# Kernel optimization log

Hardware: AMD Instinct MI355X
Metric: run time of the kernel (lower is better)

## Reference

```python
import jax, jax.numpy as jnp
import numpy as np

DIM = 768
HEADS = 12
HEAD_DIM = DIM // HEADS


def setup_inputs() -> dict:
    key = jax.random.key(0)
    ks = jax.random.split(key, 5)
    B, N = 2, 2048
    x = jax.random.normal(ks[0], (B, N, DIM), dtype=jnp.float32)
    s = 1.0 / np.sqrt(DIM)
    qkv_w = jax.random.normal(ks[1], (3 * DIM, DIM), dtype=jnp.float32) * s
    qkv_b = jnp.zeros((3 * DIM,), dtype=jnp.float32)
    proj_w = jax.random.normal(ks[2], (DIM, DIM), dtype=jnp.float32) * s
    proj_b = jnp.zeros((DIM,), dtype=jnp.float32)
    return {"x": x, "qkv_w": qkv_w, "qkv_b": qkv_b, "proj_w": proj_w, "proj_b": proj_b}


def reference(x, qkv_w, qkv_b, proj_w, proj_b):
    B, N, C = x.shape
    scale = HEAD_DIM ** -0.5
    qkv = x @ qkv_w.T + qkv_b                      # [B,N,3C]
    qkv = qkv.reshape(B, N, 3, HEADS, HEAD_DIM)
    q = qkv[:, :, 0].transpose(0, 2, 1, 3)         # [B,H,N,D]
    k = qkv[:, :, 1].transpose(0, 2, 1, 3)
    v = qkv[:, :, 2].transpose(0, 2, 1, 3)
    attn = jnp.einsum('bhnd,bhmd->bhnm', q, k) * scale
    attn = jax.nn.softmax(attn, axis=-1)
    out = jnp.einsum('bhnm,bhmd->bhnd', attn, v)   # [B,H,N,D]
    out = out.transpose(0, 2, 1, 3).reshape(B, N, C)
    return out @ proj_w.T + proj_b
```

## Files before the change

### kernel.cpp

```cpp
#include <hip/hip_runtime.h>
#include <hip/hip_bf16.h>

typedef __bf16 bf16x8 __attribute__((ext_vector_type(8)));
typedef float f32x4 __attribute__((ext_vector_type(4)));
typedef float f32x16 __attribute__((ext_vector_type(16)));

#define SEQ   2048
#define NHEAD 12
#define NBH   24
#define QSCALE 0.18033688011112042f

#define CP16(g, l) __builtin_amdgcn_global_load_lds( \
    (const __attribute__((address_space(1))) unsigned int*)(g), \
    (__attribute__((address_space(3))) unsigned int*)(l), 16, 0, 0)

__device__ __forceinline__ unsigned short f2bf(float f) {
  unsigned int u = __builtin_bit_cast(unsigned int, f);
  u += 0x7FFFu + ((u >> 16) & 1u);
  return (unsigned short)(u >> 16);
}
__device__ __forceinline__ unsigned int packbf2_trunc(float lo, float hi) {
  return __builtin_amdgcn_perm(__builtin_bit_cast(unsigned int, hi),
                               __builtin_bit_cast(unsigned int, lo), 0x07060302u);
}
__device__ __forceinline__ float vmax16(const f32x16& s) {
  float a = fmaxf(fmaxf(s[0], s[1]), fmaxf(s[2], s[3]));
  float b = fmaxf(fmaxf(s[4], s[5]), fmaxf(s[6], s[7]));
  float c = fmaxf(fmaxf(s[8], s[9]), fmaxf(s[10], s[11]));
  float d = fmaxf(fmaxf(s[12], s[13]), fmaxf(s[14], s[15]));
  return fmaxf(fmaxf(a, b), fmaxf(c, d));
}

#define NX4  786432
#define NW14 442368
__global__ __launch_bounds__(256) void cvt3_kernel(const float4* __restrict__ x,
                                                   const float4* __restrict__ w1,
                                                   const float4* __restrict__ w2,
                                                   ushort4* __restrict__ xo,
                                                   ushort4* __restrict__ w1o,
                                                   ushort4* __restrict__ w2o) {
  int i = blockIdx.x * 256 + threadIdx.x;
  const float4* s;
  ushort4* d;
  int j = i;
  if (i < NX4)               { s = x;  d = xo; }
  else if (i < NX4 + NW14)   { s = w1; d = w1o; j = i - NX4; }
  else                       { s = w2; d = w2o; j = i - (NX4 + NW14); }
  float4 v = s[j];
  ushort4 r;
  r.x = f2bf(v.x); r.y = f2bf(v.y); r.z = f2bf(v.z); r.w = f2bf(v.w);
  d[j] = r;
}

template <int BM, int BN, int MODE>
__global__ __launch_bounds__(256) void gemm_kernel(const unsigned short* __restrict__ X,
                                                   const unsigned short* __restrict__ W,
                                                   const float* __restrict__ bias,
                                                   unsigned short* __restrict__ Qb,
                                                   unsigned short* __restrict__ Kb,
                                                   unsigned short* __restrict__ Vtb,
                                                   float* __restrict__ Out) {
  constexpr int K = 768, BK = 64;
  constexpr int WM = BM / 2, WN = BN / 2;
  constexpr int MT = WM / 16, NT = WN / 16;
  __shared__ __align__(16) unsigned short Xs[BM * BK];
  __shared__ __align__(16) unsigned short Ws[BN * BK];

  const int tid = threadIdx.x;
  const int w = tid >> 6, lane = tid & 63, quad = lane >> 4, m16 = lane & 15;
  const int wm = w & 1, wn = w >> 1;
  const int row0 = blockIdx.y * BM, col0 = blockIdx.x * BN;

  f32x4 acc[MT][NT];
#pragma unroll
  for (int mt = 0; mt < MT; ++mt)
#pragma unroll
    for (int nt = 0; nt < NT; ++nt) acc[mt][nt] = (f32x4){0.f, 0.f, 0.f, 0.f};

  for (int k0 = 0; k0 < K; k0 += BK) {
    __syncthreads();
#pragma unroll
    for (int j = 0; j < BM / 32; ++j) {
      int e = tid + 256 * j, r = e >> 3, c8 = e & 7;
      CP16(X + (size_t)(row0 + r) * 768 + k0 + ((c8 ^ (r & 7)) << 3), Xs + e * 8);
    }
#pragma unroll
    for (int j = 0; j < BN / 32; ++j) {
      int e = tid + 256 * j, r = e >> 3, c8 = e & 7;
      CP16(W + (size_t)(col0 + r) * 768 + k0 + ((c8 ^ (r & 7)) << 3), Ws + e * 8);
    }
    __syncthreads();
#pragma unroll
    for (int ks = 0; ks < 2; ++ks) {
      const int sw = ((quad + 4 * ks) ^ (m16 & 7)) << 3;
      bf16x8 a[MT], b[NT];
#pragma unroll
      for (int mt = 0; mt < MT; ++mt)
        a[mt] = *(const bf16x8*)(Xs + (wm * WM + mt * 16 + m16) * BK + sw);
#pragma unroll
      for (int nt = 0; nt < NT; ++nt)
        b[nt] = *(const bf16x8*)(Ws + (wn * WN + nt * 16 + m16) * BK + sw);
#pragma unroll
      for (int mt = 0; mt < MT; ++mt)
#pragma unroll
        for (int nt = 0; nt < NT; ++nt)
          acc[mt][nt] = __builtin_amdgcn_mfma_f32_16x16x32_bf16(a[mt], b[nt], acc[mt][nt], 0, 0, 0);
    }
  }

#pragma unroll
  for (int mt = 0; mt < MT; ++mt) {
#pragma unroll
    for (int nt = 0; nt < NT; ++nt) {
      const int m0 = row0 + wm * WM + mt * 16 + quad * 4;
      const int c = col0 + wn * WN + nt * 16 + m16;
      const float bia = bias[c];
      f32x4 v = acc[mt][nt];
      if constexpr (MODE == 0) {
        const int bidx = m0 >> 11, ns = m0 & 2047;
        if (c < 1536) {
          unsigned short* dst;
          float sc;
          int cc;
          if (c < 768) { cc = c; dst = Qb; sc = QSCALE; }
          else         { cc = c - 768; dst = Kb; sc = 1.0f; }
          const int h = cc >> 6, d = cc & 63;
          unsigned short* p = dst + ((size_t)(bidx * NHEAD + h) * SEQ + ns) * 64 + d;
          p[0]   = f2bf((v[0] + bia) * sc);
          p[64]  = f2bf((v[1] + bia) * sc);
          p[128] = f2bf((v[2] + bia) * sc);
          p[192] = f2bf((v[3] + bia) * sc);
        } else {
          const int cc = c - 1536, h = cc >> 6, d = cc & 63;
          const int ns2 = (ns & ~12) | ((ns & 4) << 1) | ((ns & 8) >> 1);
          ushort4 pk;
          pk.x = f2bf(v[0] + bia); pk.y = f2bf(v[1] + bia);
          pk.z = f2bf(v[2] + bia); pk.w = f2bf(v[3] + bia);
          *(ushort4*)(Vtb + ((size_t)(bidx * NHEAD + h) * 64 + d) * SEQ + ns2) = pk;
        }
      } else {
        float* o = Out + (size_t)m0 * 768 + c;
        o[0]       = v[0] + bia;
        o[768]     = v[1] + bia;
        o[2 * 768] = v[2] + bia;
        o[3 * 768] = v[3] + bia;
      }
    }
  }
}

__global__ __launch_bounds__(128, 1) void attn_kernel(const unsigned short* __restrict__ Qb,
                                                      const unsigned short* __restrict__ Kb,
                                                      const unsigned short* __restrict__ Vtb,
                                                      unsigned short* __restrict__ Ab) {
  __shared__ __align__(16) unsigned short S[4][64 * 64];

  const int tid = threadIdx.x;
  const int w = tid >> 6, lane = tid & 63, hi = lane >> 5, l32 = lane & 31;
  const int bh = blockIdx.x % NBH, qt = blockIdx.x / NBH;
  const int bb = bh / NHEAD, h = bh % NHEAD;
  const int q0 = qt * 64 + w * 32;

  const unsigned short* Qp = Qb + (size_t)bh * SEQ * 64;
  const unsigned short* Kp = Kb + (size_t)bh * SEQ * 64;
  const unsigned short* Vp = Vtb + (size_t)bh * 64 * SEQ;

  bf16x8 qf[4];
#pragma unroll
  for (int dc = 0; dc < 4; ++dc)
    qf[dc] = *(const bf16x8*)(Qp + (size_t)(q0 + l32) * 64 + dc * 16 + hi * 8);

  const unsigned short* dsb[2][4];
#pragma unroll
  for (int t32 = 0; t32 < 2; ++t32)
#pragma unroll
    for (int c = 0; c < 4; ++c)
      dsb[t32][c] = &S[0][(t32 * 32 + l32) * 64 + ((((c << 1) | hi) ^ (l32 & 7)) << 3)];

  int koff[4], voff[4];
#pragma unroll
  for (int j = 0; j < 4; ++j) {
    const int e = tid + 128 * j, r = e >> 3, sw = ((e & 7) ^ (r & 7)) << 3;
    koff[j] = r * 64 + sw;
    voff[j] = r * SEQ + sw;
  }
  const int edst = tid * 8;

#pragma unroll
  for (int j = 0; j < 4; ++j) {
    CP16(Kp + koff[j], &S[0][edst + 1024 * j]);
    CP16(Vp + voff[j], &S[2][edst + 1024 * j]);
  }

  f32x16 o[2] = {};
  float m_i = -3.0e38f, l_i = 0.f;
  const unsigned short* Kt = Kp + 4096;
  const unsigned short* Vt = Vp + 64;

#pragma unroll 2
  for (int kt = 0; kt < 32; ++kt) {
    const int cur = kt & 1;
    __syncthreads();

    bf16x8 kf[2][4], vf[2][4];
#pragma unroll
    for (int t32 = 0; t32 < 2; ++t32)
#pragma unroll
      for (int c = 0; c < 4; ++c)
        kf[t32][c] = *(const bf16x8*)(dsb[t32][c] + cur * 4096);
#pragma unroll
    for (int dt = 0; dt < 2; ++dt)
#pragma unroll
      for (int c = 0; c < 4; ++c)
        vf[dt][c] = *(const bf16x8*)(dsb[dt][c] + 8192 + cur * 4096);

    if (kt < 31) {
#pragma unroll
      for (int j = 0; j < 4; ++j) {
        CP16(Kt + koff[j], &S[1 - cur][edst + 1024 * j]);
        CP16(Vt + voff[j], &S[3 - cur][edst + 1024 * j]);
      }
    }
    Kt += 4096;
    Vt += 64;

    __builtin_amdgcn_s_setprio(1);
    f32x16 st[2];
#pragma unroll
    for (int t32 = 0; t32 < 2; ++t32) {
      f32x16 s = {};
#pragma unroll
      for (int dc = 0; dc < 4; ++dc)
        s = __builtin_amdgcn_mfma_f32_32x32x16_bf16(kf[t32][dc], qf[dc], s, 0, 0, 0);
      st[t32] = s;
    }
    __builtin_amdgcn_s_setprio(0);

    float tmax = fmaxf(vmax16(st[0]), vmax16(st[1]));
    tmax = fmaxf(tmax, __shfl_xor(tmax, 32));
    const float mnew = fmaxf(m_i, tmax);
    const float alpha = __builtin_amdgcn_exp2f(m_i - mnew);
    unsigned int pf[2][8];
    float ts[2];
#pragma unroll
    for (int t32 = 0; t32 < 2; ++t32) {
      float pv[16];
#pragma unroll
      for (int e = 0; e < 16; ++e) pv[e] = __builtin_amdgcn_exp2f(st[t32][e] - mnew);
#pragma unroll
      for (int e2 = 0; e2 < 8; ++e2)
        pf[t32][e2] = packbf2_trunc(pv[2 * e2], pv[2 * e2 + 1]);
      const float a = (pv[0] + pv[1]) + (pv[2] + pv[3]);
      const float b = (pv[4] + pv[5]) + (pv[6] + pv[7]);
      const float c = (pv[8] + pv[9]) + (pv[10] + pv[11]);
      const float d = (pv[12] + pv[13]) + (pv[14] + pv[15]);
      ts[t32] = (a + b) + (c + d);
    }
    float ssum = ts[0] + ts[1];
    ssum += __shfl_xor(ssum, 32);
    l_i = l_i * alpha + ssum;
    m_i = mnew;
    o[0] *= alpha;
    o[1] *= alpha;

    __builtin_amdgcn_s_setprio(1);
#pragma unroll
    for (int t32 = 0; t32 < 2; ++t32) {
#pragma unroll
      for (int hh = 0; hh < 2; ++hh) {
        bf16x8 pfrag = __builtin_bit_cast(bf16x8,
            make_uint4(pf[t32][hh * 4], pf[t32][hh * 4 + 1], pf[t32][hh * 4 + 2], pf[t32][hh * 4 + 3]));
        const int cc = 2 * t32 + hh;
#pragma unroll
        for (int dt = 0; dt < 2; ++dt)
          o[dt] = __builtin_amdgcn_mfma_f32_32x32x16_bf16(vf[dt][cc], pfrag, o[dt], 0, 0, 0);
      }
    }
    __builtin_amdgcn_s_setprio(0);
  }

  const float rl = __builtin_amdgcn_rcpf(l_i);
  unsigned short* base = Ab + ((size_t)bb * SEQ + q0 + l32) * 768 + h * 64;
#pragma unroll
  for (int dt = 0; dt < 2; ++dt) {
#pragma unroll
    for (int run = 0; run < 4; ++run) {
      ushort4 pk;
      pk.x = f2bf(o[dt][run * 4 + 0] * rl);
      pk.y = f2bf(o[dt][run * 4 + 1] * rl);
      pk.z = f2bf(o[dt][run * 4 + 2] * rl);
      pk.w = f2bf(o[dt][run * 4 + 3] * rl);
      *(ushort4*)(base + dt * 32 + run * 8 + hi * 4) = pk;
    }
  }
}

extern "C" void kernel_launch(void* const* d_in, const int* in_sizes, int n_in,
                              void* d_out, int out_size, void* d_ws, size_t ws_size,
                              hipStream_t stream) {
  const float* x      = (const float*)d_in[0];
  const float* qkv_w  = (const float*)d_in[1];
  const float* qkv_b  = (const float*)d_in[2];
  const float* proj_w = (const float*)d_in[3];
  const float* proj_b = (const float*)d_in[4];
  float* out = (float*)d_out;

  unsigned short* xb  = (unsigned short*)d_ws;
  unsigned short* wqb = xb + 3145728;
  unsigned short* wpb = wqb + 1769472;
  unsigned short* Qb  = wpb + 589824;
  unsigned short* Kb  = Qb + 3145728;
  unsigned short* Vtb = Kb + 3145728;
  unsigned short* Ab  = Vtb + 3145728;

  cvt3_kernel<<<5376, 256, 0, stream>>>((const float4*)x, (const float4*)qkv_w, (const float4*)proj_w,
                                        (ushort4*)xb, (ushort4*)wqb, (ushort4*)wpb);
  gemm_kernel<128, 96, 0><<<dim3(24, 32), 256, 0, stream>>>(xb, wqb, qkv_b, Qb, Kb, Vtb, nullptr);
  attn_kernel<<<768, 128, 0, stream>>>(Qb, Kb, Vtb, Ab);
  gemm_kernel<64, 96, 1><<<dim3(8, 64), 256, 0, stream>>>(Ab, wpb, proj_b, nullptr, nullptr, nullptr, out);
}
```

Measured before the change: 171.7 us.

## Split attention over key halves into single-wave blocks with a combine kernel

The attention kernel now launches four times as many one-wave blocks. Each block processes 32 queries against half of the key sequence and reads K and V fragments straight from global memory instead of staging them through double-buffered LDS with barriers. Each half writes an unnormalized bf16 partial output plus its running max and sum, and a new combine kernel merges the two halves with rescaling. The aim is higher occupancy and more parallel work for the attention stage. In exchange it adds an extra kernel launch, extra global traffic for the partials, redundant per-wave K/V loads that now depend on cache hits, and an extra bf16 rounding of the intermediates.

```diff
diff --git a/kernel.cpp b/kernel.cpp
--- a/kernel.cpp
+++ b/kernel.cpp
@@ -18,6 +18,9 @@
   unsigned int u = __builtin_bit_cast(unsigned int, f);
   u += 0x7FFFu + ((u >> 16) & 1u);
   return (unsigned short)(u >> 16);
+}
+__device__ __forceinline__ float bfu2f(unsigned int lo16_as_hi) {
+  return __builtin_bit_cast(float, lo16_as_hi);
 }
 __device__ __forceinline__ unsigned int packbf2_trunc(float lo, float hi) {
   return __builtin_amdgcn_perm(__builtin_bit_cast(unsigned int, hi),
@@ -149,80 +152,45 @@
   }
 }
 
-__global__ __launch_bounds__(128, 1) void attn_kernel(const unsigned short* __restrict__ Qb,
-                                                      const unsigned short* __restrict__ Kb,
-                                                      const unsigned short* __restrict__ Vtb,
-                                                      unsigned short* __restrict__ Ab) {
-  __shared__ __align__(16) unsigned short S[4][64 * 64];
-
-  const int tid = threadIdx.x;
-  const int w = tid >> 6, lane = tid & 63, hi = lane >> 5, l32 = lane & 31;
-  const int bh = blockIdx.x % NBH, qt = blockIdx.x / NBH;
+__global__ __launch_bounds__(64) void attn_kernel(const unsigned short* __restrict__ Qb,
+                                                  const unsigned short* __restrict__ Kb,
+                                                  const unsigned short* __restrict__ Vtb,
+                                                  unsigned short* __restrict__ O0,
+                                                  unsigned short* __restrict__ O1,
+                                                  float2* __restrict__ ml) {
+  const int lane = threadIdx.x, hi = lane >> 5, l32 = lane & 31;
+  const int bh = blockIdx.x % NBH;
+  const int rest = blockIdx.x / NBH;
+  const int qt = rest & 63, half = rest >> 6;
   const int bb = bh / NHEAD, h = bh % NHEAD;
-  const int q0 = qt * 64 + w * 32;
+  const int q0 = qt * 32;
 
   const unsigned short* Qp = Qb + (size_t)bh * SEQ * 64;
-  const unsigned short* Kp = Kb + (size_t)bh * SEQ * 64;
-  const unsigned short* Vp = Vtb + (size_t)bh * 64 * SEQ;
-
   bf16x8 qf[4];
 #pragma unroll
   for (int dc = 0; dc < 4; ++dc)
     qf[dc] = *(const bf16x8*)(Qp + (size_t)(q0 + l32) * 64 + dc * 16 + hi * 8);
 
-  const unsigned short* dsb[2][4];
-#pragma unroll
-  for (int t32 = 0; t32 < 2; ++t32)
-#pragma unroll
-    for (int c = 0; c < 4; ++c)
-      dsb[t32][c] = &S[0][(t32 * 32 + l32) * 64 + ((((c << 1) | hi) ^ (l32 & 7)) << 3)];
-
-  int koff[4], voff[4];
-#pragma unroll
-  for (int j = 0; j < 4; ++j) {
-    const int e = tid + 128 * j, r = e >> 3, sw = ((e & 7) ^ (r & 7)) << 3;
-    koff[j] = r * 64 + sw;
-    voff[j] = r * SEQ + sw;
-  }
-  const int edst = tid * 8;
-
-#pragma unroll
-  for (int j = 0; j < 4; ++j) {
-    CP16(Kp + koff[j], &S[0][edst + 1024 * j]);
-    CP16(Vp + voff[j], &S[2][edst + 1024 * j]);
-  }
+  const int kt0 = half * 16;
+  const unsigned short* k0p = Kb + (size_t)bh * SEQ * 64 + (size_t)(kt0 * 64 + l32) * 64 + hi * 8;
+  const unsigned short* k1p = k0p + 32 * 64;
+  const unsigned short* v0p = Vtb + (size_t)bh * 64 * SEQ + (size_t)l32 * SEQ + kt0 * 64 + hi * 8;
+  const unsigned short* v1p = v0p + (size_t)32 * SEQ;
 
   f32x16 o[2] = {};
   float m_i = -3.0e38f, l_i = 0.f;
-  const unsigned short* Kt = Kp + 4096;
-  const unsigned short* Vt = Vp + 64;
 
 #pragma unroll 2
-  for (int kt = 0; kt < 32; ++kt) {
-    const int cur = kt & 1;
-    __syncthreads();
-
+  for (int kt = 0; kt < 16; ++kt) {
     bf16x8 kf[2][4], vf[2][4];
 #pragma unroll
-    for (int t32 = 0; t32 < 2; ++t32)
-#pragma unroll
-      for (int c = 0; c < 4; ++c)
-        kf[t32][c] = *(const bf16x8*)(dsb[t32][c] + cur * 4096);
-#pragma unroll
-    for (int dt = 0; dt < 2; ++dt)
-#pragma unroll
-      for (int c = 0; c < 4; ++c)
-        vf[dt][c] = *(const bf16x8*)(dsb[dt][c] + 8192 + cur * 4096);
-
-    if (kt < 31) {
-#pragma unroll
-      for (int j = 0; j < 4; ++j) {
-        CP16(Kt + koff[j], &S[1 - cur][edst + 1024 * j]);
-        CP16(Vt + voff[j], &S[3 - cur][edst + 1024 * j]);
-      }
-    }
-    Kt += 4096;
-    Vt += 64;
+    for (int c = 0; c < 4; ++c) {
+      kf[0][c] = *(const bf16x8*)(k0p + c * 16);
+      kf[1][c] = *(const bf16x8*)(k1p + c * 16);
+      vf[0][c] = *(const bf16x8*)(v0p + c * 16);
+      vf[1][c] = *(const bf16x8*)(v1p + c * 16);
+    }
+    k0p += 4096; k1p += 4096; v0p += 64; v1p += 64;
 
     __builtin_amdgcn_s_setprio(1);
     f32x16 st[2];
@@ -240,59 +208,92 @@
     tmax = fmaxf(tmax, __shfl_xor(tmax, 32));
     const float mnew = fmaxf(m_i, tmax);
     const float alpha = __builtin_amdgcn_exp2f(m_i - mnew);
-    unsigned int pf[2][8];
+    m_i = mnew;
+    l_i *= alpha;
+    o[0] *= alpha;
+    o[1] *= alpha;
+
     float ts[2];
 #pragma unroll
     for (int t32 = 0; t32 < 2; ++t32) {
       float pv[16];
 #pragma unroll
       for (int e = 0; e < 16; ++e) pv[e] = __builtin_amdgcn_exp2f(st[t32][e] - mnew);
+      unsigned int pf[8];
 #pragma unroll
       for (int e2 = 0; e2 < 8; ++e2)
-        pf[t32][e2] = packbf2_trunc(pv[2 * e2], pv[2 * e2 + 1]);
+        pf[e2] = packbf2_trunc(pv[2 * e2], pv[2 * e2 + 1]);
       const float a = (pv[0] + pv[1]) + (pv[2] + pv[3]);
       const float b = (pv[4] + pv[5]) + (pv[6] + pv[7]);
       const float c = (pv[8] + pv[9]) + (pv[10] + pv[11]);
       const float d = (pv[12] + pv[13]) + (pv[14] + pv[15]);
       ts[t32] = (a + b) + (c + d);
-    }
-    float ssum = ts[0] + ts[1];
-    ssum += __shfl_xor(ssum, 32);
-    l_i = l_i * alpha + ssum;
-    m_i = mnew;
-    o[0] *= alpha;
-    o[1] *= alpha;
-
-    __builtin_amdgcn_s_setprio(1);
-#pragma unroll
-    for (int t32 = 0; t32 < 2; ++t32) {
+      __builtin_amdgcn_s_setprio(1);
 #pragma unroll
       for (int hh = 0; hh < 2; ++hh) {
         bf16x8 pfrag = __builtin_bit_cast(bf16x8,
-            make_uint4(pf[t32][hh * 4], pf[t32][hh * 4 + 1], pf[t32][hh * 4 + 2], pf[t32][hh * 4 + 3]));
+            make_uint4(pf[hh * 4], pf[hh * 4 + 1], pf[hh * 4 + 2], pf[hh * 4 + 3]));
         const int cc = 2 * t32 + hh;
 #pragma unroll
         for (int dt = 0; dt < 2; ++dt)
           o[dt] = __builtin_amdgcn_mfma_f32_32x32x16_bf16(vf[dt][cc], pfrag, o[dt], 0, 0, 0);
       }
-    }
-    __builtin_amdgcn_s_setprio(0);
-  }
-
-  const float rl = __builtin_amdgcn_rcpf(l_i);
-  unsigned short* base = Ab + ((size_t)bb * SEQ + q0 + l32) * 768 + h * 64;
+      __builtin_amdgcn_s_setprio(0);
+    }
+    float ssum = ts[0] + ts[1];
+    ssum += __shfl_xor(ssum, 32);
+    l_i += ssum;
+  }
+
+  unsigned short* base = (half ? O1 : O0) + ((size_t)bb * SEQ + q0 + l32) * 768 + h * 64;
 #pragma unroll
   for (int dt = 0; dt < 2; ++dt) {
 #pragma unroll
     for (int run = 0; run < 4; ++run) {
       ushort4 pk;
-      pk.x = f2bf(o[dt][run * 4 + 0] * rl);
-      pk.y = f2bf(o[dt][run * 4 + 1] * rl);
-      pk.z = f2bf(o[dt][run * 4 + 2] * rl);
-      pk.w = f2bf(o[dt][run * 4 + 3] * rl);
+      pk.x = f2bf(o[dt][run * 4 + 0]);
+      pk.y = f2bf(o[dt][run * 4 + 1]);
+      pk.z = f2bf(o[dt][run * 4 + 2]);
+      pk.w = f2bf(o[dt][run * 4 + 3]);
       *(ushort4*)(base + dt * 32 + run * 8 + hi * 4) = pk;
     }
   }
+  if (hi == 0)
+    ml[(size_t)half * (NBH * SEQ) + bh * SEQ + q0 + l32] = make_float2(m_i, l_i);
+}
+
+__global__ __launch_bounds__(256) void combine_kernel(unsigned short* __restrict__ O0,
+                                                      const unsigned short* __restrict__ O1,
+                                                      const float2* __restrict__ ml) {
+  const int gid = blockIdx.x * 256 + threadIdx.x;
+  const int t = gid / 48, ci = gid - t * 48;
+  const int ch0 = ci * 16, h = ch0 >> 6;
+  const int mlrow = ((t >> 11) * NHEAD + h) * SEQ + (t & 2047);
+  const float2 ml0 = ml[mlrow], ml1 = ml[NBH * SEQ + mlrow];
+  const float m = fmaxf(ml0.x, ml1.x);
+  const float a0 = __builtin_amdgcn_exp2f(ml0.x - m);
+  const float a1 = __builtin_amdgcn_exp2f(ml1.x - m);
+  const float rl = __builtin_amdgcn_rcpf(a0 * ml0.y + a1 * ml1.y);
+  const float s0 = a0 * rl, s1 = a1 * rl;
+  unsigned short* p0 = O0 + (size_t)t * 768 + ch0;
+  const unsigned short* p1 = O1 + (size_t)t * 768 + ch0;
+  uint4 x[2], y[2];
+  x[0] = *(const uint4*)p0;       x[1] = *(const uint4*)(p0 + 8);
+  y[0] = *(const uint4*)p1;       y[1] = *(const uint4*)(p1 + 8);
+#pragma unroll
+  for (int q = 0; q < 2; ++q) {
+    unsigned int* xu = (unsigned int*)&x[q];
+    const unsigned int* yu = (const unsigned int*)&y[q];
+#pragma unroll
+    for (int e = 0; e < 4; ++e) {
+      const unsigned int u0 = xu[e], u1 = yu[e];
+      const float lo = bfu2f(u0 << 16) * s0 + bfu2f(u1 << 16) * s1;
+      const float hi = bfu2f(u0 & 0xFFFF0000u) * s0 + bfu2f(u1 & 0xFFFF0000u) * s1;
+      xu[e] = ((unsigned int)f2bf(hi) << 16) | f2bf(lo);
+    }
+  }
+  *(uint4*)p0 = x[0];
+  *(uint4*)(p0 + 8) = x[1];
 }
 
 extern "C" void kernel_launch(void* const* d_in, const int* in_sizes, int n_in,
@@ -316,6 +317,7 @@
   cvt3_kernel<<<5376, 256, 0, stream>>>((const float4*)x, (const float4*)qkv_w, (const float4*)proj_w,
                                         (ushort4*)xb, (ushort4*)wqb, (ushort4*)wpb);
   gemm_kernel<128, 96, 0><<<dim3(24, 32), 256, 0, stream>>>(xb, wqb, qkv_b, Qb, Kb, Vtb, nullptr);
-  attn_kernel<<<768, 128, 0, stream>>>(Qb, Kb, Vtb, Ab);
+  attn_kernel<<<3072, 64, 0, stream>>>(Qb, Kb, Vtb, Ab, xb, (float2*)wqb);
+  combine_kernel<<<768, 256, 0, stream>>>(Ab, xb, (const float2*)wqb);
   gemm_kernel<64, 96, 1><<<dim3(8, 64), 256, 0, stream>>>(Ab, wpb, proj_b, nullptr, nullptr, nullptr, out);
 }
```

New measurement: 213.1 us. 1.24x slower.

## Split attention KV range in halves, double queries per wave, add combine kernel

Applied to the files above, without the earlier changes.

Each attention wave now handles 64 query rows (two 32-row sub-tiles) that share the same K/V fragments loaded from LDS, halving LDS traffic per query. Work is split along the key dimension into two halves, keeping the block count at 768. Each half writes unnormalized bf16 partial outputs plus per-row (max, sum) to repurposed workspace buffers. A new combine kernel merges the halves with log-sum-exp rescaling. Occupancy is hinted at two blocks per CU. The cost is an extra kernel pass over two activation-sized buffers, higher register pressure, and an added bf16 rounding of unnormalized partials.

```diff
diff --git a/kernel.cpp b/kernel.cpp
--- a/kernel.cpp
+++ b/kernel.cpp
@@ -18,6 +18,9 @@
   unsigned int u = __builtin_bit_cast(unsigned int, f);
   u += 0x7FFFu + ((u >> 16) & 1u);
   return (unsigned short)(u >> 16);
+}
+__device__ __forceinline__ float bfu2f(unsigned int lo16_as_hi) {
+  return __builtin_bit_cast(float, lo16_as_hi);
 }
 __device__ __forceinline__ unsigned int packbf2_trunc(float lo, float hi) {
   return __builtin_amdgcn_perm(__builtin_bit_cast(unsigned int, hi),
@@ -149,26 +152,32 @@
   }
 }
 
-__global__ __launch_bounds__(128, 1) void attn_kernel(const unsigned short* __restrict__ Qb,
+__global__ __launch_bounds__(128, 2) void attn_kernel(const unsigned short* __restrict__ Qb,
                                                       const unsigned short* __restrict__ Kb,
                                                       const unsigned short* __restrict__ Vtb,
-                                                      unsigned short* __restrict__ Ab) {
+                                                      unsigned short* __restrict__ O0,
+                                                      unsigned short* __restrict__ O1,
+                                                      float2* __restrict__ ml) {
   __shared__ __align__(16) unsigned short S[4][64 * 64];
 
   const int tid = threadIdx.x;
   const int w = tid >> 6, lane = tid & 63, hi = lane >> 5, l32 = lane & 31;
-  const int bh = blockIdx.x % NBH, qt = blockIdx.x / NBH;
+  const int bh = blockIdx.x % NBH;
+  const int rest = blockIdx.x / NBH;
+  const int qt = rest & 15, half = rest >> 4;
   const int bb = bh / NHEAD, h = bh % NHEAD;
-  const int q0 = qt * 64 + w * 32;
+  const int q0 = qt * 128 + w * 64;
 
   const unsigned short* Qp = Qb + (size_t)bh * SEQ * 64;
-  const unsigned short* Kp = Kb + (size_t)bh * SEQ * 64;
-  const unsigned short* Vp = Vtb + (size_t)bh * 64 * SEQ;
-
-  bf16x8 qf[4];
-#pragma unroll
-  for (int dc = 0; dc < 4; ++dc)
-    qf[dc] = *(const bf16x8*)(Qp + (size_t)(q0 + l32) * 64 + dc * 16 + hi * 8);
+  const unsigned short* Kp = Kb + (size_t)bh * SEQ * 64 + (size_t)half * 16 * 4096;
+  const unsigned short* Vp = Vtb + (size_t)bh * 64 * SEQ + half * 1024;
+
+  bf16x8 qf[2][4];
+#pragma unroll
+  for (int qs = 0; qs < 2; ++qs)
+#pragma unroll
+    for (int dc = 0; dc < 4; ++dc)
+      qf[qs][dc] = *(const bf16x8*)(Qp + (size_t)(q0 + qs * 32 + l32) * 64 + dc * 16 + hi * 8);
 
   const unsigned short* dsb[2][4];
 #pragma unroll
@@ -192,13 +201,14 @@
     CP16(Vp + voff[j], &S[2][edst + 1024 * j]);
   }
 
-  f32x16 o[2] = {};
-  float m_i = -3.0e38f, l_i = 0.f;
+  f32x16 o[2][2] = {};
+  float m_i[2] = {-3.0e38f, -3.0e38f};
+  float l_i[2] = {0.f, 0.f};
   const unsigned short* Kt = Kp + 4096;
   const unsigned short* Vt = Vp + 64;
 
 #pragma unroll 2
-  for (int kt = 0; kt < 32; ++kt) {
+  for (int kt = 0; kt < 16; ++kt) {
     const int cur = kt & 1;
     __syncthreads();
 
@@ -214,7 +224,7 @@
       for (int c = 0; c < 4; ++c)
         vf[dt][c] = *(const bf16x8*)(dsb[dt][c] + 8192 + cur * 4096);
 
-    if (kt < 31) {
+    if (kt < 15) {
 #pragma unroll
       for (int j = 0; j < 4; ++j) {
         CP16(Kt + koff[j], &S[1 - cur][edst + 1024 * j]);
@@ -225,74 +235,167 @@
     Vt += 64;
 
     __builtin_amdgcn_s_setprio(1);
-    f32x16 st[2];
+    f32x16 st0[2];
 #pragma unroll
     for (int t32 = 0; t32 < 2; ++t32) {
       f32x16 s = {};
 #pragma unroll
       for (int dc = 0; dc < 4; ++dc)
-        s = __builtin_amdgcn_mfma_f32_32x32x16_bf16(kf[t32][dc], qf[dc], s, 0, 0, 0);
-      st[t32] = s;
+        s = __builtin_amdgcn_mfma_f32_32x32x16_bf16(kf[t32][dc], qf[0][dc], s, 0, 0, 0);
+      st0[t32] = s;
     }
     __builtin_amdgcn_s_setprio(0);
 
-    float tmax = fmaxf(vmax16(st[0]), vmax16(st[1]));
-    tmax = fmaxf(tmax, __shfl_xor(tmax, 32));
-    const float mnew = fmaxf(m_i, tmax);
-    const float alpha = __builtin_amdgcn_exp2f(m_i - mnew);
-    unsigned int pf[2][8];
-    float ts[2];
+    unsigned int pf0[2][8];
+    {
+      float tmax = fmaxf(vmax16(st0[0]), vmax16(st0[1]));
+      tmax = fmaxf(tmax, __shfl_xor(tmax, 32));
+      const float mnew = fmaxf(m_i[0], tmax);
+      const float alpha = __builtin_amdgcn_exp2f(m_i[0] - mnew);
+      m_i[0] = mnew;
+      float ts[2];
+#pragma unroll
+      for (int t32 = 0; t32 < 2; ++t32) {
+        float pv[16];
+#pragma unroll
+        for (int e = 0; e < 16; ++e) pv[e] = __builtin_amdgcn_exp2f(st0[t32][e] - mnew);
+#pragma unroll
+        for (int e2 = 0; e2 < 8; ++e2)
+          pf0[t32][e2] = packbf2_trunc(pv[2 * e2], pv[2 * e2 + 1]);
+        const float a = (pv[0] + pv[1]) + (pv[2] + pv[3]);
+        const float b = (pv[4] + pv[5]) + (pv[6] + pv[7]);
+        const float c = (pv[8] + pv[9]) + (pv[10] + pv[11]);
+        const float d = (pv[12] + pv[13]) + (pv[14] + pv[15]);
+        ts[t32] = (a + b) + (c + d);
+      }
+      float ssum = ts[0] + ts[1];
+      ssum += __shfl_xor(ssum, 32);
+      l_i[0] = l_i[0] * alpha + ssum;
+      o[0][0] *= alpha;
+      o[0][1] *= alpha;
+    }
+
+    __builtin_amdgcn_s_setprio(1);
+    f32x16 st1[2];
 #pragma unroll
     for (int t32 = 0; t32 < 2; ++t32) {
-      float pv[16];
-#pragma unroll
-      for (int e = 0; e < 16; ++e) pv[e] = __builtin_amdgcn_exp2f(st[t32][e] - mnew);
-#pragma unroll
-      for (int e2 = 0; e2 < 8; ++e2)
-        pf[t32][e2] = packbf2_trunc(pv[2 * e2], pv[2 * e2 + 1]);
-      const float a = (pv[0] + pv[1]) + (pv[2] + pv[3]);
-      const float b = (pv[4] + pv[5]) + (pv[6] + pv[7]);
-      const float c = (pv[8] + pv[9]) + (pv[10] + pv[11]);
-      const float d = (pv[12] + pv[13]) + (pv[14] + pv[15]);
-      ts[t32] = (a + b) + (c + d);
-    }
-    float ssum = ts[0] + ts[1];
-    ssum += __shfl_xor(ssum, 32);
-    l_i = l_i * alpha + ssum;
-    m_i = mnew;
-    o[0] *= alpha;
-    o[1] *= alpha;
-
-    __builtin_amdgcn_s_setprio(1);
-#pragma unroll
-    for (int t32 = 0; t32 < 2; ++t32) {
+      f32x16 s = {};
+#pragma unroll
+      for (int dc = 0; dc < 4; ++dc)
+        s = __builtin_amdgcn_mfma_f32_32x32x16_bf16(kf[t32][dc], qf[1][dc], s, 0, 0, 0);
+      st1[t32] = s;
+    }
+
+#pragma unroll
+    for (int t32 = 0; t32 < 2; ++t32)
 #pragma unroll
       for (int hh = 0; hh < 2; ++hh) {
         bf16x8 pfrag = __builtin_bit_cast(bf16x8,
-            make_uint4(pf[t32][hh * 4], pf[t32][hh * 4 + 1], pf[t32][hh * 4 + 2], pf[t32][hh * 4 + 3]));
+            make_uint4(pf0[t32][hh * 4], pf0[t32][hh * 4 + 1], pf0[t32][hh * 4 + 2], pf0[t32][hh * 4 + 3]));
         const int cc = 2 * t32 + hh;
 #pragma unroll
         for (int dt = 0; dt < 2; ++dt)
-          o[dt] = __builtin_amdgcn_mfma_f32_32x32x16_bf16(vf[dt][cc], pfrag, o[dt], 0, 0, 0);
-      }
-    }
+          o[0][dt] = __builtin_amdgcn_mfma_f32_32x32x16_bf16(vf[dt][cc], pfrag, o[0][dt], 0, 0, 0);
+      }
     __builtin_amdgcn_s_setprio(0);
-  }
-
-  const float rl = __builtin_amdgcn_rcpf(l_i);
-  unsigned short* base = Ab + ((size_t)bb * SEQ + q0 + l32) * 768 + h * 64;
-#pragma unroll
-  for (int dt = 0; dt < 2; ++dt) {
-#pragma unroll
-    for (int run = 0; run < 4; ++run) {
-      ushort4 pk;
-      pk.x = f2bf(o[dt][run * 4 + 0] * rl);
-      pk.y = f2bf(o[dt][run * 4 + 1] * rl);
-      pk.z = f2bf(o[dt][run * 4 + 2] * rl);
-      pk.w = f2bf(o[dt][run * 4 + 3] * rl);
-      *(ushort4*)(base + dt * 32 + run * 8 + hi * 4) = pk;
-    }
-  }
+
+    unsigned int pf1[2][8];
+    {
+      float tmax = fmaxf(vmax16(st1[0]), vmax16(st1[1]));
+      tmax = fmaxf(tmax, __shfl_xor(tmax, 32));
+      const float mnew = fmaxf(m_i[1], tmax);
+      const float alpha = __builtin_amdgcn_exp2f(m_i[1] - mnew);
+      m_i[1] = mnew;
+      float ts[2];
+#pragma unroll
+      for (int t32 = 0; t32 < 2; ++t32) {
+        float pv[16];
+#pragma unroll
+        for (int e = 0; e < 16; ++e) pv[e] = __builtin_amdgcn_exp2f(st1[t32][e] - mnew);
+#pragma unroll
+        for (int e2 = 0; e2 < 8; ++e2)
+          pf1[t32][e2] = packbf2_trunc(pv[2 * e2], pv[2 * e2 + 1]);
+        const float a = (pv[0] + pv[1]) + (pv[2] + pv[3]);
+        const float b = (pv[4] + pv[5]) + (pv[6] + pv[7]);
+        const float c = (pv[8] + pv[9]) + (pv[10] + pv[11]);
+        const float d = (pv[12] + pv[13]) + (pv[14] + pv[15]);
+        ts[t32] = (a + b) + (c + d);
+      }
+      float ssum = ts[0] + ts[1];
+      ssum += __shfl_xor(ssum, 32);
+      l_i[1] = l_i[1] * alpha + ssum;
+      o[1][0] *= alpha;
+      o[1][1] *= alpha;
+    }
+
+    __builtin_amdgcn_s_setprio(1);
+#pragma unroll
+    for (int t32 = 0; t32 < 2; ++t32)
+#pragma unroll
+      for (int hh = 0; hh < 2; ++hh) {
+        bf16x8 pfrag = __builtin_bit_cast(bf16x8,
+            make_uint4(pf1[t32][hh * 4], pf1[t32][hh * 4 + 1], pf1[t32][hh * 4 + 2], pf1[t32][hh * 4 + 3]));
+        const int cc = 2 * t32 + hh;
+#pragma unroll
+        for (int dt = 0; dt < 2; ++dt)
+          o[1][dt] = __builtin_amdgcn_mfma_f32_32x32x16_bf16(vf[dt][cc], pfrag, o[1][dt], 0, 0, 0);
+      }
+    __builtin_amdgcn_s_setprio(0);
+  }
+
+  unsigned short* Od = half ? O1 : O0;
+#pragma unroll
+  for (int qs = 0; qs < 2; ++qs) {
+    unsigned short* base = Od + ((size_t)bb * SEQ + q0 + qs * 32 + l32) * 768 + h * 64;
+#pragma unroll
+    for (int dt = 0; dt < 2; ++dt) {
+#pragma unroll
+      for (int run = 0; run < 4; ++run) {
+        ushort4 pk;
+        pk.x = f2bf(o[qs][dt][run * 4 + 0]);
+        pk.y = f2bf(o[qs][dt][run * 4 + 1]);
+        pk.z = f2bf(o[qs][dt][run * 4 + 2]);
+        pk.w = f2bf(o[qs][dt][run * 4 + 3]);
+        *(ushort4*)(base + dt * 32 + run * 8 + hi * 4) = pk;
+      }
+    }
+    if (hi == 0)
+      ml[(size_t)half * (NBH * SEQ) + bh * SEQ + q0 + qs * 32 + l32] = make_float2(m_i[qs], l_i[qs]);
+  }
+}
+
+__global__ __launch_bounds__(256) void combine_kernel(unsigned short* __restrict__ O0,
+                                                      const unsigned short* __restrict__ O1,
+                                                      const float2* __restrict__ ml) {
+  const int gid = blockIdx.x * 256 + threadIdx.x;
+  const int t = gid / 48, ci = gid - t * 48;
+  const int ch0 = ci * 16, h = ch0 >> 6;
+  const int mlrow = ((t >> 11) * NHEAD + h) * SEQ + (t & 2047);
+  const float2 ml0 = ml[mlrow], ml1 = ml[NBH * SEQ + mlrow];
+  const float m = fmaxf(ml0.x, ml1.x);
+  const float a0 = __builtin_amdgcn_exp2f(ml0.x - m);
+  const float a1 = __builtin_amdgcn_exp2f(ml1.x - m);
+  const float rl = __builtin_amdgcn_rcpf(a0 * ml0.y + a1 * ml1.y);
+  const float s0 = a0 * rl, s1 = a1 * rl;
+  unsigned short* p0 = O0 + (size_t)t * 768 + ch0;
+  const unsigned short* p1 = O1 + (size_t)t * 768 + ch0;
+  uint4 x[2], y[2];
+  x[0] = *(const uint4*)p0;       x[1] = *(const uint4*)(p0 + 8);
+  y[0] = *(const uint4*)p1;       y[1] = *(const uint4*)(p1 + 8);
+#pragma unroll
+  for (int q = 0; q < 2; ++q) {
+    unsigned int* xu = (unsigned int*)&x[q];
+    const unsigned int* yu = (const unsigned int*)&y[q];
+#pragma unroll
+    for (int e = 0; e < 4; ++e) {
+      const unsigned int u0 = xu[e], u1 = yu[e];
+      const float lo = bfu2f(u0 << 16) * s0 + bfu2f(u1 << 16) * s1;
+      const float hi = bfu2f(u0 & 0xFFFF0000u) * s0 + bfu2f(u1 & 0xFFFF0000u) * s1;
+      xu[e] = ((unsigned int)f2bf(hi) << 16) | f2bf(lo);
+    }
+  }
+  *(uint4*)p0 = x[0];
+  *(uint4*)(p0 + 8) = x[1];
 }
 
 extern "C" void kernel_launch(void* const* d_in, const int* in_sizes, int n_in,
@@ -316,6 +419,7 @@
   cvt3_kernel<<<5376, 256, 0, stream>>>((const float4*)x, (const float4*)qkv_w, (const float4*)proj_w,
                                         (ushort4*)xb, (ushort4*)wqb, (ushort4*)wpb);
   gemm_kernel<128, 96, 0><<<dim3(24, 32), 256, 0, stream>>>(xb, wqb, qkv_b, Qb, Kb, Vtb, nullptr);
-  attn_kernel<<<768, 128, 0, stream>>>(Qb, Kb, Vtb, Ab);
+  attn_kernel<<<768, 128, 0, stream>>>(Qb, Kb, Vtb, Ab, xb, (float2*)wqb);
+  combine_kernel<<<768, 256, 0, stream>>>(Ab, xb, (const float2*)wqb);
   gemm_kernel<64, 96, 1><<<dim3(8, 64), 256, 0, stream>>>(Ab, wpb, proj_b, nullptr, nullptr, nullptr, out);
 }
```

Result: slower. 197.8 us (+15.2%).
